# Kernel optimization log

Measured on AMD Instinct MI355X. Metric: run time of the kernel, lower is better.

The kernel has to match this reference:

```python
import jax, jax.numpy as jnp
import numpy as np


def _rgcn_layer(x, rel, adj, W, b):
    # x: [B, N, De], rel: [B, R, Dr], adj: [B, R, N, N]
    # Torch loop: for each r, bmm(adj[:, r], cat([x, rel[:, r] broadcast], -1)), then cat over r.
    B, N, De = x.shape
    R, Dr = rel.shape[1], rel.shape[2]
    h = jnp.concatenate(
        [jnp.broadcast_to(x[:, None], (B, R, N, De)),
         jnp.broadcast_to(rel[:, :, None], (B, R, N, Dr))],
        axis=-1)                                   # [B, R, N, De+Dr]
    # supports, with relation axis placed before features to match torch cat order
    s = jnp.einsum('brmn,brnd->bmrd', adj, h)      # [B, N, R, De+Dr]
    s = s.reshape(B, N, R * (De + Dr))             # [B, N, R*(De+Dr)]
    return s @ W.T + b                             # [B, N, out_dim]


def setup_inputs() -> dict:
    key = jax.random.key(0)
    ks = jax.random.split(key, 6)
    B, N, R = 16, 1024, 10
    De, Dr, H = 64, 32, 64
    cat_in = (De + Dr) * R  # 960
    node_features = jax.random.normal(ks[0], (B, N, De), dtype=jnp.float32)
    relation_features = jax.random.normal(ks[1], (B, R, Dr), dtype=jnp.float32)
    adj = jax.random.uniform(ks[2], (B, R, N, N), dtype=jnp.float32)
    scale0 = np.sqrt(6.0 / (cat_in + H)).astype(np.float32)  # xavier_uniform
    W0 = jax.random.uniform(ks[3], (H, cat_in), minval=-scale0, maxval=scale0, dtype=jnp.float32)
    b0 = jnp.zeros((H,), dtype=jnp.float32)
    W1 = jax.random.uniform(ks[4], (H, cat_in), minval=-scale0, maxval=scale0, dtype=jnp.float32)
    b1 = jnp.zeros((H,), dtype=jnp.float32)
    return {"node_features": node_features, "relation_features": relation_features,
            "adj": adj, "W0": W0, "b0": b0, "W1": W1, "b1": b1}


def reference(node_features, relation_features, adj, W0, b0, W1, b1):
    # StackedRelationalGraphConvolution.forward, 2 layers, no highway,
    # real_valued_graph=False (ReLU), dropout_rate=0 (inference no-op).
    x = jax.nn.relu(_rgcn_layer(node_features, relation_features, adj, W0, b0))
    x = jax.nn.relu(_rgcn_layer(x, relation_features, adj, W1, b1))
    return x
```

## Files before the change

### kernel.cpp

```cpp
#include <hip/hip_runtime.h>
#include <hip/hip_bf16.h>


typedef __bf16 bf16x8 __attribute__((ext_vector_type(8)));
typedef float  f32x4  __attribute__((ext_vector_type(4)));

__global__ __launch_bounds__(256)
void rgcn_prep(const float* __restrict__ x, const float* __restrict__ rel,
               const float* __restrict__ W, __bf16* __restrict__ yt) {
    const int r = blockIdx.y, b = blockIdx.z;
    const int br = b * 10 + r;

    __shared__ float csh[64];
    if (threadIdx.x < 64) {
        const int h = threadIdx.x;
        const float* rp = rel + (size_t)br * 32;
        const float* wp = W + (size_t)h * 960 + r * 96 + 64;
        float a = 0.f;
#pragma unroll
        for (int d = 0; d < 32; ++d) a += rp[d] * wp[d];
        csh[h] = a;
    }
    __syncthreads();

    const int n = blockIdx.x * 256 + threadIdx.x;
    float xr[64];
    const float* xp = x + ((size_t)b * 1024 + n) * 64;
#pragma unroll
    for (int j = 0; j < 16; ++j) {
        const float4 v = *(const float4*)(xp + j * 4);
        xr[j * 4 + 0] = v.x; xr[j * 4 + 1] = v.y;
        xr[j * 4 + 2] = v.z; xr[j * 4 + 3] = v.w;
    }

    const float* wbase = W + r * 96;
    __bf16* yb = yt + ((size_t)br << 16) + n;
    for (int h = 0; h < 64; ++h) {
        float acc = csh[h];
        const float* wr = wbase + (size_t)h * 960;
#pragma unroll
        for (int d = 0; d < 64; ++d) acc += xr[d] * wr[d];
        yb[(size_t)h << 10] = (__bf16)acc;
    }
}

template<bool FUSE>
__global__ __launch_bounds__(256, 4)
void rgcn_main(const float* __restrict__ adj, const __bf16* __restrict__ yt,
               float* __restrict__ partial, const float* __restrict__ bias,
               float* __restrict__ dst) {
    const int w = threadIdx.x >> 6, lane = threadIdx.x & 63;
    const int g = lane >> 4, lm = lane & 15;

#define LDNT(p, o) __builtin_nontemporal_load((const f32x4*)((p) + (o)))

    if constexpr (!FUSE) {
        const int br = blockIdx.x;
        const int mtile = blockIdx.y;
        const int mbase = mtile * 128 + w * 32;

        const float*  a0 = adj + (((size_t)br * 1024 + mbase + lm) << 10) + g * 8;
        const float*  a1 = a0 + (16 << 10);
        const __bf16* y0 = yt + ((size_t)br << 16) + (lm << 10) + g * 8;

        f32x4 acc[2][4] = {};
        f32x4 c00 = LDNT(a0, 0), c01 = LDNT(a0, 4);
        f32x4 c10 = LDNT(a1, 0), c11 = LDNT(a1, 4);

#define STEP(N0)                                                               \
        {                                                                      \
            bf16x8 av0, av1;                                                   \
            _Pragma("unroll")                                                  \
            for (int j = 0; j < 4; ++j) {                                      \
                av0[j] = (__bf16)c00[j]; av0[4 + j] = (__bf16)c01[j];          \
                av1[j] = (__bf16)c10[j]; av1[4 + j] = (__bf16)c11[j];          \
            }                                                                  \
            _Pragma("unroll")                                                  \
            for (int hf = 0; hf < 4; ++hf) {                                   \
                const bf16x8 bv = *(const bf16x8*)(y0 + hf * 16384 + (N0));    \
                acc[0][hf] = __builtin_amdgcn_mfma_f32_16x16x32_bf16(av0, bv, acc[0][hf], 0, 0, 0); \
                acc[1][hf] = __builtin_amdgcn_mfma_f32_16x16x32_bf16(av1, bv, acc[1][hf], 0, 0, 0); \
            }                                                                  \
        }

        for (int n0 = 0; n0 < 992; n0 += 32) {
            const f32x4 p00 = LDNT(a0, n0 + 32), p01 = LDNT(a0, n0 + 36);
            const f32x4 p10 = LDNT(a1, n0 + 32), p11 = LDNT(a1, n0 + 36);
            STEP(n0)
            c00 = p00; c01 = p01; c10 = p10; c11 = p11;
        }
        STEP(992)

        float* pb = partial + ((size_t)br << 16);
#pragma unroll
        for (int mf = 0; mf < 2; ++mf)
#pragma unroll
            for (int hf = 0; hf < 4; ++hf)
#pragma unroll
                for (int reg = 0; reg < 4; ++reg) {
                    const int m = mbase + mf * 16 + g * 4 + reg;
                    const int h = hf * 16 + lm;
                    pb[((size_t)m << 6) + h] = acc[mf][hf][reg];
                }
    } else {
        const int b = blockIdx.x;
        const int mtile = blockIdx.y;
        const int mbase = mtile * 128 + w * 32;

        f32x4 acc[2][4] = {};
        for (int r = 0; r < 10; ++r) {
            const int br = b * 10 + r;
            const float*  a0 = adj + (((size_t)br * 1024 + mbase + lm) << 10) + g * 8;
            const float*  a1 = a0 + (16 << 10);
            const __bf16* y0 = yt + ((size_t)br << 16) + (lm << 10) + g * 8;
            f32x4 c00 = LDNT(a0, 0), c01 = LDNT(a0, 4);
            f32x4 c10 = LDNT(a1, 0), c11 = LDNT(a1, 4);
            for (int n0 = 0; n0 < 992; n0 += 32) {
                const f32x4 p00 = LDNT(a0, n0 + 32), p01 = LDNT(a0, n0 + 36);
                const f32x4 p10 = LDNT(a1, n0 + 32), p11 = LDNT(a1, n0 + 36);
                STEP(n0)
                c00 = p00; c01 = p01; c10 = p10; c11 = p11;
            }
            STEP(992)
        }
        float bvals[4];
#pragma unroll
        for (int hf = 0; hf < 4; ++hf) bvals[hf] = bias[hf * 16 + lm];
        float* db = dst + (((size_t)b * 1024 + mbase) << 6);
#pragma unroll
        for (int mf = 0; mf < 2; ++mf)
#pragma unroll
            for (int hf = 0; hf < 4; ++hf)
#pragma unroll
                for (int reg = 0; reg < 4; ++reg) {
                    const int m = mf * 16 + g * 4 + reg;
                    const int h = hf * 16 + lm;
                    db[((size_t)m << 6) + h] = fmaxf(acc[mf][hf][reg] + bvals[hf], 0.f);
                }
    }
#undef STEP
#undef LDNT
}

__global__ __launch_bounds__(256)
void rgcn_epi(const float* __restrict__ partial, const float* __restrict__ bias,
              float* __restrict__ dst) {
    const size_t i = (size_t)blockIdx.x * 256 + threadIdx.x;
    const size_t off = i * 4;
    const size_t b = off >> 16;
    const size_t inner = off & 65535;
    f32x4 s = {};
#pragma unroll
    for (int p = 0; p < 10; ++p)
        s += *(const f32x4*)(partial + (((b * 10 + p) << 16) | inner));
    const f32x4 bv = *(const f32x4*)(bias + (int)(off & 63));
#pragma unroll
    for (int j = 0; j < 4; ++j) s[j] = fmaxf(s[j] + bv[j], 0.f);
    *(f32x4*)(dst + off) = s;
}

extern "C" void kernel_launch(void* const* d_in, const int* in_sizes, int n_in,
                              void* d_out, int out_size, void* d_ws, size_t ws_size,
                              hipStream_t stream) {
    const float* x   = (const float*)d_in[0];
    const float* rel = (const float*)d_in[1];
    const float* adj = (const float*)d_in[2];
    const float* W0  = (const float*)d_in[3];
    const float* b0  = (const float*)d_in[4];
    const float* W1  = (const float*)d_in[5];
    const float* b1  = (const float*)d_in[6];
    float* out = (float*)d_out;

    char* ws = (char*)d_ws;
    __bf16* Yt  = (__bf16*)ws;
    float* x2   = (float*)(ws + 20971520);
    float* part = (float*)(ws + 25165824);
    const bool big = ws_size >= 67108864;

    for (int layer = 0; layer < 2; ++layer) {
        const float* xin  = layer ? x2 : x;
        const float* W    = layer ? W1 : W0;
        const float* bias = layer ? b1 : b0;
        float* dst        = layer ? out : x2;

        rgcn_prep<<<dim3(4, 10, 16), 256, 0, stream>>>(xin, rel, W, Yt);
        if (big) {
            rgcn_main<false><<<dim3(160, 8), 256, 0, stream>>>(adj, Yt, part, nullptr, nullptr);
            rgcn_epi<<<1024, 256, 0, stream>>>(part, bias, dst);
        } else {
            rgcn_main<true><<<dim3(16, 8), 256, 0, stream>>>(adj, Yt, nullptr, bias, dst);
        }
    }
}
```

Measured before the change: 631.3 us.

## Stage Y tiles in swizzled LDS and use 512-thread blocks with deeper adj prefetch

The main kernel now copies each relation's full bf16 Y slice (64x1024) into shared memory with an XOR swizzle, so B-operand reads come from LDS rather than global memory. Each wave handles 16 rows instead of 32, eight waves per block, and adj rows are streamed as 8-wide vectors through a 4-deep register prefetch ring. A middle workspace tier is added that splits relations across 2 blocks with 5 partials. The 128KB LDS footprint limits occupancy to one block per CU, and the added staging and syncs cost some time per relation.

```diff
diff --git a/kernel.cpp b/kernel.cpp
--- a/kernel.cpp
+++ b/kernel.cpp
@@ -4,6 +4,7 @@
 
 typedef __bf16 bf16x8 __attribute__((ext_vector_type(8)));
 typedef float  f32x4  __attribute__((ext_vector_type(4)));
+typedef float  f32x8  __attribute__((ext_vector_type(8)));
 
 __global__ __launch_bounds__(256)
 void rgcn_prep(const float* __restrict__ x, const float* __restrict__ rel,
@@ -44,104 +45,90 @@
     }
 }
 
-template<bool FUSE>
-__global__ __launch_bounds__(256, 4)
+template<int NRI, bool FUSE>
+__global__ __launch_bounds__(512)
 void rgcn_main(const float* __restrict__ adj, const __bf16* __restrict__ yt,
                float* __restrict__ partial, const float* __restrict__ bias,
                float* __restrict__ dst) {
-    const int w = threadIdx.x >> 6, lane = threadIdx.x & 63;
+    constexpr int RSPAN = 10 / NRI;
+    const int bx = blockIdx.x;
+    const int b  = bx / RSPAN, r0 = bx % RSPAN;
+    const int mtile = blockIdx.y;
+    const int tid = threadIdx.x;
+    const int w = tid >> 6, lane = tid & 63;
     const int g = lane >> 4, lm = lane & 15;
+    const int mloc = mtile * 128 + w * 16 + lm;
+    const int msk = (lm & 7) << 3;
 
-#define LDNT(p, o) __builtin_nontemporal_load((const f32x4*)((p) + (o)))
+    __shared__ __bf16 sh[65536];
 
-    if constexpr (!FUSE) {
-        const int br = blockIdx.x;
-        const int mtile = blockIdx.y;
-        const int mbase = mtile * 128 + w * 32;
+    f32x4 acc[4] = {};
 
-        const float*  a0 = adj + (((size_t)br * 1024 + mbase + lm) << 10) + g * 8;
-        const float*  a1 = a0 + (16 << 10);
-        const __bf16* y0 = yt + ((size_t)br << 16) + (lm << 10) + g * 8;
+    for (int i = 0; i < NRI; ++i) {
+        const int r = r0 + i * RSPAN;
+        const int br = b * 10 + r;
 
-        f32x4 acc[2][4] = {};
-        f32x4 c00 = LDNT(a0, 0), c01 = LDNT(a0, 4);
-        f32x4 c10 = LDNT(a1, 0), c11 = LDNT(a1, 4);
+        if (i) __syncthreads();
+        const __bf16* ysrc = yt + ((size_t)br << 16);
+#pragma unroll
+        for (int it = 0; it < 16; ++it) {
+            const int e = (it * 512 + tid) * 8;
+            const uint4 v = *(const uint4*)(ysrc + e);
+            const int h = e >> 10, nn = e & 1023;
+            *(uint4*)(sh + (h << 10) + (nn ^ ((h & 7) << 3))) = v;
+        }
+        __syncthreads();
 
-#define STEP(N0)                                                               \
-        {                                                                      \
-            bf16x8 av0, av1;                                                   \
-            _Pragma("unroll")                                                  \
-            for (int j = 0; j < 4; ++j) {                                      \
-                av0[j] = (__bf16)c00[j]; av0[4 + j] = (__bf16)c01[j];          \
-                av1[j] = (__bf16)c10[j]; av1[4 + j] = (__bf16)c11[j];          \
-            }                                                                  \
-            _Pragma("unroll")                                                  \
-            for (int hf = 0; hf < 4; ++hf) {                                   \
-                const bf16x8 bv = *(const bf16x8*)(y0 + hf * 16384 + (N0));    \
-                acc[0][hf] = __builtin_amdgcn_mfma_f32_16x16x32_bf16(av0, bv, acc[0][hf], 0, 0, 0); \
-                acc[1][hf] = __builtin_amdgcn_mfma_f32_16x16x32_bf16(av1, bv, acc[1][hf], 0, 0, 0); \
-            }                                                                  \
+        const float* arow = adj + (((size_t)(br * 1024 + mloc)) << 10) + g * 8;
+        f32x8 pf[4];
+#pragma unroll
+        for (int p = 0; p < 4; ++p)
+            pf[p] = __builtin_nontemporal_load((const f32x8*)(arow + p * 32));
+
+#pragma unroll 4
+        for (int n0 = 0; n0 < 1024; n0 += 32) {
+            const int slot = (n0 >> 5) & 3;
+            const f32x8 cur = pf[slot];
+            pf[slot] = __builtin_nontemporal_load(
+                (const f32x8*)(arow + ((n0 + 128) & 1023)));
+            bf16x8 av;
+#pragma unroll
+            for (int j = 0; j < 8; ++j) av[j] = (__bf16)cur[j];
+            const int nc = n0 + g * 8;
+#pragma unroll
+            for (int hf = 0; hf < 4; ++hf) {
+                const int h = hf * 16 + lm;
+                const bf16x8 bv = *(const bf16x8*)(sh + (h << 10) + (nc ^ msk));
+                acc[hf] = __builtin_amdgcn_mfma_f32_16x16x32_bf16(av, bv, acc[hf], 0, 0, 0);
+            }
         }
+    }
 
-        for (int n0 = 0; n0 < 992; n0 += 32) {
-            const f32x4 p00 = LDNT(a0, n0 + 32), p01 = LDNT(a0, n0 + 36);
-            const f32x4 p10 = LDNT(a1, n0 + 32), p11 = LDNT(a1, n0 + 36);
-            STEP(n0)
-            c00 = p00; c01 = p01; c10 = p10; c11 = p11;
+    if (FUSE) {
+        float* db = dst + (((size_t)b << 10) + mtile * 128 + w * 16) * 64;
+#pragma unroll
+        for (int hf = 0; hf < 4; ++hf) {
+            const float bb = bias[hf * 16 + lm];
+#pragma unroll
+            for (int reg = 0; reg < 4; ++reg) {
+                const int ml = g * 4 + reg;
+                db[(size_t)ml * 64 + hf * 16 + lm] = fmaxf(acc[hf][reg] + bb, 0.f);
+            }
         }
-        STEP(992)
-
-        float* pb = partial + ((size_t)br << 16);
+    } else {
+        float* pb = partial + (((size_t)(r0 * 16 + b)) << 16)
+                  + (size_t)(mtile * 128 + w * 16) * 64;
 #pragma unroll
-        for (int mf = 0; mf < 2; ++mf)
+        for (int hf = 0; hf < 4; ++hf)
 #pragma unroll
-            for (int hf = 0; hf < 4; ++hf)
-#pragma unroll
-                for (int reg = 0; reg < 4; ++reg) {
-                    const int m = mbase + mf * 16 + g * 4 + reg;
-                    const int h = hf * 16 + lm;
-                    pb[((size_t)m << 6) + h] = acc[mf][hf][reg];
-                }
-    } else {
-        const int b = blockIdx.x;
-        const int mtile = blockIdx.y;
-        const int mbase = mtile * 128 + w * 32;
-
-        f32x4 acc[2][4] = {};
-        for (int r = 0; r < 10; ++r) {
-            const int br = b * 10 + r;
-            const float*  a0 = adj + (((size_t)br * 1024 + mbase + lm) << 10) + g * 8;
-            const float*  a1 = a0 + (16 << 10);
-            const __bf16* y0 = yt + ((size_t)br << 16) + (lm << 10) + g * 8;
-            f32x4 c00 = LDNT(a0, 0), c01 = LDNT(a0, 4);
-            f32x4 c10 = LDNT(a1, 0), c11 = LDNT(a1, 4);
-            for (int n0 = 0; n0 < 992; n0 += 32) {
-                const f32x4 p00 = LDNT(a0, n0 + 32), p01 = LDNT(a0, n0 + 36);
-                const f32x4 p10 = LDNT(a1, n0 + 32), p11 = LDNT(a1, n0 + 36);
-                STEP(n0)
-                c00 = p00; c01 = p01; c10 = p10; c11 = p11;
+            for (int reg = 0; reg < 4; ++reg) {
+                const int ml = g * 4 + reg;
+                pb[(size_t)ml * 64 + hf * 16 + lm] = acc[hf][reg];
             }
-            STEP(992)
-        }
-        float bvals[4];
-#pragma unroll
-        for (int hf = 0; hf < 4; ++hf) bvals[hf] = bias[hf * 16 + lm];
-        float* db = dst + (((size_t)b * 1024 + mbase) << 6);
-#pragma unroll
-        for (int mf = 0; mf < 2; ++mf)
-#pragma unroll
-            for (int hf = 0; hf < 4; ++hf)
-#pragma unroll
-                for (int reg = 0; reg < 4; ++reg) {
-                    const int m = mf * 16 + g * 4 + reg;
-                    const int h = hf * 16 + lm;
-                    db[((size_t)m << 6) + h] = fmaxf(acc[mf][hf][reg] + bvals[hf], 0.f);
-                }
     }
-#undef STEP
-#undef LDNT
 }
 
+template<int NP>
 __global__ __launch_bounds__(256)
 void rgcn_epi(const float* __restrict__ partial, const float* __restrict__ bias,
               float* __restrict__ dst) {
@@ -151,8 +138,8 @@
     const size_t inner = off & 65535;
     f32x4 s = {};
 #pragma unroll
-    for (int p = 0; p < 10; ++p)
-        s += *(const f32x4*)(partial + (((b * 10 + p) << 16) | inner));
+    for (int p = 0; p < NP; ++p)
+        s += *(const f32x4*)(partial + (((size_t)(p * 16) + b) << 16) + inner);
     const f32x4 bv = *(const f32x4*)(bias + (int)(off & 63));
 #pragma unroll
     for (int j = 0; j < 4; ++j) s[j] = fmaxf(s[j] + bv[j], 0.f);
@@ -175,7 +162,8 @@
     __bf16* Yt  = (__bf16*)ws;
     float* x2   = (float*)(ws + 20971520);
     float* part = (float*)(ws + 25165824);
-    const bool big = ws_size >= 67108864;
+    const size_t need1 = 25165824u + 41943040u;
+    const size_t need2 = 25165824u + 20971520u;
 
     for (int layer = 0; layer < 2; ++layer) {
         const float* xin  = layer ? x2 : x;
@@ -184,11 +172,14 @@
         float* dst        = layer ? out : x2;
 
         rgcn_prep<<<dim3(4, 10, 16), 256, 0, stream>>>(xin, rel, W, Yt);
-        if (big) {
-            rgcn_main<false><<<dim3(160, 8), 256, 0, stream>>>(adj, Yt, part, nullptr, nullptr);
-            rgcn_epi<<<1024, 256, 0, stream>>>(part, bias, dst);
+        if (ws_size >= need1) {
+            rgcn_main<1, false><<<dim3(160, 8), 512, 0, stream>>>(adj, Yt, part, nullptr, nullptr);
+            rgcn_epi<10><<<1024, 256, 0, stream>>>(part, bias, dst);
+        } else if (ws_size >= need2) {
+            rgcn_main<2, false><<<dim3(80, 8), 512, 0, stream>>>(adj, Yt, part, nullptr, nullptr);
+            rgcn_epi<5><<<1024, 256, 0, stream>>>(part, bias, dst);
         } else {
-            rgcn_main<true><<<dim3(16, 8), 256, 0, stream>>>(adj, Yt, nullptr, bias, dst);
+            rgcn_main<10, true><<<dim3(16, 8), 512, 0, stream>>>(adj, Yt, nullptr, bias, dst);
         }
     }
 }
```

Measured after the change: 547.0 us. -13.3%, faster.
